# Kernel optimization log

Hardware: AMD Instinct MI355X
Metric: run time of the kernel (lower is better)

## Reference

```python
import jax, jax.numpy as jnp
import numpy as np

ORDER = 1024
U_SIZE = 128
Y_SIZE = 128
N_STEPS = 32768


def setup_inputs() -> dict:
    key = jax.random.key(0)
    k0, k1, k2, k3, k4 = jax.random.split(key, 5)
    inp = jax.random.normal(k0, (N_STEPS, U_SIZE), dtype=jnp.float32)
    # A scaled to spectral radius ~0.9 so the 32k-step recurrence is stable.
    A_w = jax.random.normal(k1, (ORDER, ORDER), dtype=jnp.float32) * (0.9 / np.sqrt(ORDER))
    B_w = jax.random.normal(k2, (ORDER, U_SIZE), dtype=jnp.float32) / np.sqrt(U_SIZE)
    C_w = jax.random.normal(k3, (Y_SIZE, ORDER), dtype=jnp.float32) / np.sqrt(ORDER)
    D_w = jax.random.normal(k4, (Y_SIZE, U_SIZE), dtype=jnp.float32) / np.sqrt(U_SIZE)
    return {"inp": inp, "A_w": A_w, "B_w": B_w, "C_w": C_w, "D_w": D_w}


def reference(inp, A_w, B_w, C_w, D_w):
    u_size = B_w.shape[1]
    order = A_w.shape[0]
    # Faithful to torch: input.reshape(u_size, -1), then column t is u at step t.
    us = inp.reshape(u_size, -1).T  # (N, u_size)
    x0 = jnp.zeros((order,), dtype=inp.dtype)

    def step(x, u):
        y = C_w @ x + D_w @ u          # (y_size,)
        x_next = A_w @ x + B_w @ u     # (order,)
        return x_next, y

    _, ys = jax.lax.scan(step, x0, us)
    return ys  # (N, y_size)
```

## Files before the change

kernel.cpp:

```cpp
#include <hip/hip_runtime.h>
#include <hip/hip_bf16.h>


#define NSTEPS 32768
#define LTRUNC 64
#define NDBLK  (LTRUNC + 1)
#define KTOT   (NDBLK * 128)
#define SPLITK 2

typedef __attribute__((ext_vector_type(8))) short short8;
typedef __attribute__((ext_vector_type(4))) float f32x4;
typedef __hip_bfloat16 bf16;

#define ME 1048576
#define O_AHR 0
#define O_ALR (1*ME)
#define O_AHC (2*ME)
#define O_ALC (3*ME)
#define O_XPH (4*ME)
#define O_XPL (5*ME)
#define O_XQH (6*ME)
#define O_XQL (7*ME)
#define O_YPH (8*ME)
#define O_YPL (9*ME)
#define O_YQH (10*ME)
#define O_YQL (11*ME)
#define O_GH  (12*ME)
#define O_GL  (14*ME)
#define O_RTH (16*ME)
#define O_RTL (O_RTH + 917504)
#define O_KBT (O_RTL + 917504)
#define O_UBF (O_KBT + 128*KTOT)

__device__ __forceinline__ void gload16(const void* g, void* l) {
  __builtin_amdgcn_global_load_lds(
      (const __attribute__((address_space(1))) void*)g,
      (__attribute__((address_space(3))) void*)l, 16, 0, 0);
}

__device__ __forceinline__ void split1(float x, bf16& h, bf16& l) {
  h = __float2bfloat16(x);
  l = __float2bfloat16(x - __bfloat162float(h));
}

__global__ __launch_bounds__(256) void prep(
    const float* __restrict__ inp, const float* __restrict__ Aw,
    const float* __restrict__ Bw, const float* __restrict__ Cw,
    const float* __restrict__ Dw, bf16* __restrict__ W, float* __restrict__ out)
{
  __shared__ float buf[128 * 65];
  const int tid = threadIdx.x;
  const int bid = blockIdx.x;

  if (bid < 512) {
    const int t0 = bid << 6;
#pragma unroll
    for (int i = 0; i < 32; ++i) {
      const int e = i * 256 + tid, sl = e >> 6, tl = e & 63;
      buf[sl * 65 + tl] = inp[(size_t)sl * NSTEPS + t0 + tl];
    }
    __syncthreads();
    bf16* Ubf = W + O_UBF;
#pragma unroll
    for (int i = 0; i < 32; ++i) {
      const int e = i * 256 + tid, tl = e >> 7, sl = e & 127;
      Ubf[(size_t)(LTRUNC + t0 + tl) * 128 + sl] = __float2bfloat16(buf[sl * 65 + tl]);
    }
  } else if (bid < 768) {
    const int base = (bid - 512) * 4096;
    bf16* hi = W + O_AHR; bf16* lo = W + O_ALR;
#pragma unroll
    for (int i = 0; i < 4; ++i) {
      const int e = base + i * 1024 + tid * 4;
      const float4 v = *reinterpret_cast<const float4*>(Aw + e);
      const float vv[4] = {v.x, v.y, v.z, v.w};
#pragma unroll
      for (int j = 0; j < 4; ++j) { bf16 h, l; split1(vv[j], h, l); hi[e+j] = h; lo[e+j] = l; }
    }
  } else if (bid < 1024) {
    const int idx = bid - 768;
    const int r0 = (idx >> 4) << 6, c0 = (idx & 15) << 6;
#pragma unroll
    for (int i = 0; i < 16; ++i) {
      const int e = i * 256 + tid, rl = e >> 6, cl = e & 63;
      buf[rl * 65 + cl] = Aw[(size_t)(r0 + rl) * 1024 + c0 + cl];
    }
    __syncthreads();
    bf16* hi = W + O_AHC; bf16* lo = W + O_ALC;
#pragma unroll
    for (int i = 0; i < 16; ++i) {
      const int e = i * 256 + tid, cl = e >> 6, rl = e & 63;
      bf16 h, l; split1(buf[rl * 65 + cl], h, l);
      hi[(size_t)(c0 + cl) * 1024 + r0 + rl] = h;
      lo[(size_t)(c0 + cl) * 1024 + r0 + rl] = l;
    }
  } else if (bid < 1056) {
    const int base = (bid - 1024) * 4096;
    bf16* hi = W + O_GH; bf16* lo = W + O_GL;
#pragma unroll
    for (int i = 0; i < 4; ++i) {
      const int e = base + i * 1024 + tid * 4;
      const float4 v = *reinterpret_cast<const float4*>(Cw + e);
      const float vv[4] = {v.x, v.y, v.z, v.w};
#pragma unroll
      for (int j = 0; j < 4; ++j) { bf16 h, l; split1(vv[j], h, l); hi[e+j] = h; lo[e+j] = l; }
    }
  } else if (bid < 1088) {
    const int idx = bid - 1056;
    const int r0 = (idx >> 1) << 6, c0 = (idx & 1) << 6;
#pragma unroll
    for (int i = 0; i < 16; ++i) {
      const int e = i * 256 + tid, rl = e >> 6, cl = e & 63;
      buf[rl * 65 + cl] = Bw[(size_t)(r0 + rl) * 128 + c0 + cl];
    }
    __syncthreads();
    bf16* hi = W + O_RTH; bf16* lo = W + O_RTL;
#pragma unroll
    for (int i = 0; i < 16; ++i) {
      const int e = i * 256 + tid, cl = e >> 6, rl = e & 63;
      bf16 h, l; split1(buf[rl * 65 + cl], h, l);
      hi[(size_t)(c0 + cl) * 1024 + r0 + rl] = h;
      lo[(size_t)(c0 + cl) * 1024 + r0 + rl] = l;
    }
  } else if (bid < 1092) {
    bf16* kb = W + O_KBT;
    const int e0 = (bid - 1088) * 4096 + tid * 16;
#pragma unroll
    for (int j = 0; j < 16; ++j) {
      const int e = e0 + j, r = e >> 7, s = e & 127;
      kb[(size_t)r * KTOT + s] = __float2bfloat16(Dw[e]);
    }
  } else if (bid < 1094) {
    bf16* Ubf = W + O_UBF;
    const int e = ((bid - 1092) * 256 + tid) * 16;
    short8 z = {0,0,0,0,0,0,0,0};
    *reinterpret_cast<short8*>(Ubf + e) = z;
    *reinterpret_cast<short8*>(Ubf + e + 8) = z;
  } else {
    float4* o4 = reinterpret_cast<float4*>(out);
    const int base = (bid - 1094) * 4096;
    const float4 z = {0.f, 0.f, 0.f, 0.f};
#pragma unroll
    for (int i = 0; i < 16; ++i) o4[base + i * 256 + tid] = z;
  }
}

struct Job { int ah, al, bh, bl, oh, ol, oth, otl, mt, nt, dbase; };
__device__ const Job JOBS[15] = {
  {O_AHR,O_ALR,O_AHC,O_ALC, O_XPH,O_XPL, O_YPH,O_YPL, 8,8,-1},
  {O_GH, O_GL, O_AHC,O_ALC, O_GH+131072,O_GL+131072, -1,-1, 1,8,-1},
  {O_XPH,O_XPL,O_YPH,O_YPL, O_XQH,O_XQL, O_YQH,O_YQL, 8,8,-1},
  {O_GH, O_GL, O_YPH,O_YPL, O_GH+262144,O_GL+262144, -1,-1, 2,8,-1},
  {O_XQH,O_XQL,O_YQH,O_YQL, O_XPH,O_XPL, O_YPH,O_YPL, 8,8,-1},
  {O_GH, O_GL, O_YQH,O_YQL, O_GH+524288,O_GL+524288, -1,-1, 4,8,-1},
  {O_XPH,O_XPL,O_YPH,O_YPL, O_XQH,O_XQL, O_YQH,O_YQL, 8,8,-1},
  {O_GH, O_GL, O_YPH,O_YPL, O_GH+1048576,O_GL+1048576, -1,-1, 8,8,-1},
  {O_XQH,O_XQL,O_YQH,O_YQL, O_XPH,O_XPL, -1,-1, 8,8,-1},
  {O_RTH,O_RTL,O_XQH,O_XQL, O_RTH+131072,O_RTL+131072, -1,-1, 1,8,-1},
  {O_GH,O_GL, O_RTH,        O_RTL,        O_KBT,0, -1,-1, 16,1, 1},
  {O_RTH,O_RTL,O_XPH,O_XPL, O_RTH+262144,O_RTL+262144, -1,-1, 2,8,-1},
  {O_GH,O_GL, O_RTH+131072, O_RTL+131072, O_KBT,0, -1,-1, 16,1, 17},
  {O_GH,O_GL, O_RTH+262144, O_RTL+262144, O_KBT,0, -1,-1, 16,1, 33},
  {O_GH,O_GL, O_RTH+393216, O_RTL+393216, O_KBT,0, -1,-1, 16,1, 49},
};
__device__ const int LVL[8] = {0,2,4,6,8,11,13,15};

__global__ __launch_bounds__(256) void chain_lvl(bf16* __restrict__ ws, int lvl)
{
  __shared__ __align__(16) char smem[131072];
  const int tid = threadIdx.x, lane = tid & 63, wave = tid >> 6;
  const int wm = wave & 1, wn = wave >> 1, l15 = lane & 15, lk = lane >> 4;
  const int srow = tid >> 3, sc8 = (tid & 7) << 3;
  const int g8 = (((tid & 7) ^ (srow & 7)) << 3);
  const int ca0 = ((lk ^ (l15 & 7)) << 3);
  const int ca1 = (((4 + lk) ^ (l15 & 7)) << 3);

  int idx = blockIdx.x;
  int j = LVL[lvl];
  const int je = LVL[lvl + 1];
  while (j < je && idx >= JOBS[j].mt * JOBS[j].nt) { idx -= JOBS[j].mt * JOBS[j].nt; ++j; }
  if (j >= je) return;
  const Job job = JOBS[j];
  const int my = idx / job.nt, nx = idx - my * job.nt;
  const int m0 = my << 7, n0 = nx << 7;
  const bf16* Ah = ws + job.ah; const bf16* Al = ws + job.al;
  const bf16* Bh = ws + job.bh; const bf16* Bl = ws + job.bl;
  f32x4 acc[4][4] = {};

  if (job.dbase >= 0) {
    auto stageK = [&](int ks, int buf) {
      char* base = smem + buf * 32768;
      const int k0 = ks << 6;
#pragma unroll
      for (int p = 0; p < 4; ++p) {
        const int row = (p << 5) + srow;
        const int loff = row * 128 + (sc8 << 1);
        gload16(Ah + (size_t)(m0 + row) * 1024 + k0 + g8, base + loff);
        gload16(Bh + (size_t)(n0 + row) * 1024 + k0 + g8, base + 16384 + loff);
      }
    };
    stageK(0, 0);
    for (int ks = 0; ks < 16; ++ks) {
      if (ks + 1 < 16) {
        stageK(ks + 1, (ks + 1) & 1);
        asm volatile("s_waitcnt vmcnt(8)" ::: "memory");
      } else {
        asm volatile("s_waitcnt vmcnt(0)" ::: "memory");
      }
      __builtin_amdgcn_s_barrier();
      __builtin_amdgcn_sched_barrier(0);
      {
        char* base = smem + (ks & 1) * 32768;
        const bf16* pAh = (const bf16*)(base);
        const bf16* pBh = (const bf16*)(base + 16384);
#pragma unroll
        for (int kh = 0; kh < 2; ++kh) {
          const int cb = kh ? ca1 : ca0;
          short8 ah[4], bh[4];
#pragma unroll
          for (int mi = 0; mi < 4; ++mi)
            ah[mi] = *reinterpret_cast<const short8*>(pAh + ((wm << 6) + (mi << 4) + l15) * 64 + cb);
#pragma unroll
          for (int ni = 0; ni < 4; ++ni)
            bh[ni] = *reinterpret_cast<const short8*>(pBh + ((wn << 6) + (ni << 4) + l15) * 64 + cb);
#pragma unroll
          for (int mi = 0; mi < 4; ++mi)
#pragma unroll
            for (int ni = 0; ni < 4; ++ni)
              acc[mi][ni] = __builtin_amdgcn_mfma_f32_16x16x32_bf16(ah[mi], bh[ni], acc[mi][ni], 0, 0, 0);
        }
      }
      __builtin_amdgcn_sched_barrier(0);
      __builtin_amdgcn_s_barrier();
    }
    bf16* kb = ws + job.oh;
    const int d = job.dbase + my;
#pragma unroll
    for (int mi = 0; mi < 4; ++mi)
#pragma unroll
      for (int ni = 0; ni < 4; ++ni) {
        const int cl = (wn << 6) + (ni << 4) + l15;
#pragma unroll
        for (int rg = 0; rg < 4; ++rg) {
          const int rl = (wm << 6) + (mi << 4) + (lk << 2) + rg;
          kb[(size_t)rl * KTOT + (size_t)d * 128 + cl] = __float2bfloat16(acc[mi][ni][rg]);
        }
      }
    return;
  }

  auto stage = [&](int ks, int buf) {
    char* base = smem + buf * 65536;
    const int k0 = ks << 6;
#pragma unroll
    for (int p = 0; p < 4; ++p) {
      const int row = (p << 5) + srow;
      const int loff = row * 128 + (sc8 << 1);
      const size_t aoff = (size_t)(m0 + row) * 1024 + k0 + g8;
      const size_t boff = (size_t)(n0 + row) * 1024 + k0 + g8;
      gload16(Ah + aoff, base + loff);
      gload16(Al + aoff, base + 16384 + loff);
      gload16(Bh + boff, base + 32768 + loff);
      gload16(Bl + boff, base + 49152 + loff);
    }
  };

  stage(0, 0);
  for (int ks = 0; ks < 16; ++ks) {
    if (ks + 1 < 16) {
      stage(ks + 1, (ks + 1) & 1);
      asm volatile("s_waitcnt vmcnt(16)" ::: "memory");
    } else {
      asm volatile("s_waitcnt vmcnt(0)" ::: "memory");
    }
    __builtin_amdgcn_s_barrier();
    __builtin_amdgcn_sched_barrier(0);
    {
      char* base = smem + (ks & 1) * 65536;
      const bf16* pAh = (const bf16*)(base);
      const bf16* pAl = (const bf16*)(base + 16384);
      const bf16* pBh = (const bf16*)(base + 32768);
      const bf16* pBl = (const bf16*)(base + 49152);
#pragma unroll
      for (int kh = 0; kh < 2; ++kh) {
        const int cb = kh ? ca1 : ca0;
        short8 ah[4], al[4], bh[4], bl[4];
#pragma unroll
        for (int mi = 0; mi < 4; ++mi) {
          const int r = ((wm << 6) + (mi << 4) + l15) * 64 + cb;
          ah[mi] = *reinterpret_cast<const short8*>(pAh + r);
          al[mi] = *reinterpret_cast<const short8*>(pAl + r);
        }
#pragma unroll
        for (int ni = 0; ni < 4; ++ni) {
          const int r = ((wn << 6) + (ni << 4) + l15) * 64 + cb;
          bh[ni] = *reinterpret_cast<const short8*>(pBh + r);
          bl[ni] = *reinterpret_cast<const short8*>(pBl + r);
        }
#pragma unroll
        for (int mi = 0; mi < 4; ++mi)
#pragma unroll
          for (int ni = 0; ni < 4; ++ni) {
            acc[mi][ni] = __builtin_amdgcn_mfma_f32_16x16x32_bf16(ah[mi], bh[ni], acc[mi][ni], 0, 0, 0);
            acc[mi][ni] = __builtin_amdgcn_mfma_f32_16x16x32_bf16(ah[mi], bl[ni], acc[mi][ni], 0, 0, 0);
            acc[mi][ni] = __builtin_amdgcn_mfma_f32_16x16x32_bf16(al[mi], bh[ni], acc[mi][ni], 0, 0, 0);
          }
      }
    }
    __builtin_amdgcn_sched_barrier(0);
    __builtin_amdgcn_s_barrier();
  }

  {
    bf16* oh = ws + job.oh; bf16* ol = ws + job.ol;
#pragma unroll
    for (int mi = 0; mi < 4; ++mi)
#pragma unroll
      for (int ni = 0; ni < 4; ++ni) {
        const int cl = (wn << 6) + (ni << 4) + l15;
#pragma unroll
        for (int rg = 0; rg < 4; ++rg) {
          const int rl = (wm << 6) + (mi << 4) + (lk << 2) + rg;
          bf16 h, l; split1(acc[mi][ni][rg], h, l);
          oh[(size_t)(m0 + rl) * 1024 + n0 + cl] = h;
          ol[(size_t)(m0 + rl) * 1024 + n0 + cl] = l;
        }
      }
    if (job.oth >= 0) {
      float* tT = (float*)smem;
      __syncthreads();
#pragma unroll
      for (int mi = 0; mi < 4; ++mi)
#pragma unroll
        for (int ni = 0; ni < 4; ++ni) {
          const int cl = (wn << 6) + (ni << 4) + l15;
#pragma unroll
          for (int rg = 0; rg < 4; ++rg) {
            const int rl = (wm << 6) + (mi << 4) + (lk << 2) + rg;
            tT[rl * 129 + cl] = acc[mi][ni][rg];
          }
        }
      __syncthreads();
      bf16* yh = ws + job.oth; bf16* yl = ws + job.otl;
#pragma unroll
      for (int i = 0; i < 64; ++i) {
        const int e = i * 256 + tid, yr = e >> 7, yc = e & 127;
        bf16 h, l; split1(tT[yc * 129 + yr], h, l);
        yh[(size_t)(n0 + yr) * 1024 + m0 + yc] = h;
        yl[(size_t)(n0 + yr) * 1024 + m0 + yc] = l;
      }
    }
  }
}

__global__ __launch_bounds__(256) void conv_mfma(
    const bf16* __restrict__ Ubf, const bf16* __restrict__ Kbt, float* __restrict__ out)
{
  __shared__ __align__(16) char smem[73728];
  const int tid = threadIdx.x;
  const int t0 = blockIdx.x << 7;
  const int y = blockIdx.y;
  const int lane = tid & 63, wave = tid >> 6;
  const int wm = wave & 1, wn = wave >> 1;
  const int l15 = lane & 15, lk = lane >> 4;
  const int srow = tid >> 3, sc8 = (tid & 7) << 3;
  const int g8 = (((tid & 7) ^ (srow & 7)) << 3);
  const int ca0 = ((lk ^ (l15 & 7)) << 3);
  const int ca1 = (((4 + lk) ^ (l15 & 7)) << 3);
  const int d_hi = y ? LTRUNC : 32;
  const int sb = y ? 66 : 0, se = y ? 130 : 66;
  bf16* U = (bf16*)smem;
  bf16* Bs0 = (bf16*)(smem + 40960);
  bf16* Bs1 = (bf16*)(smem + 57344);
  f32x4 acc[4][4] = {};

  const long u0 = (long)LTRUNC + t0 - d_hi;
#pragma unroll
  for (int i = 0; i < 10; ++i) {
    const int idx = i * 256 + tid;
    const int r = idx >> 4, c = idx & 15;
    gload16(Ubf + (size_t)(u0 + r) * 128 + ((c ^ (r & 15)) << 3), smem + idx * 16);
  }

  auto stageB = [&](int it, bf16* Bbuf) {
    const int kk0 = it << 6;
#pragma unroll
    for (int p = 0; p < 4; ++p) {
      const int row = (p << 5) + srow;
      gload16(Kbt + (size_t)row * KTOT + kk0 + g8, Bbuf + row * 64 + sc8);
    }
  };

  stageB(sb, Bs0);
  int cur = 0;
  for (int it = sb; it < se; ++it) {
    if (it + 1 < se) {
      stageB(it + 1, cur ? Bs0 : Bs1);
      asm volatile("s_waitcnt vmcnt(4)" ::: "memory");
    } else {
      asm volatile("s_waitcnt vmcnt(0)" ::: "memory");
    }
    __builtin_amdgcn_s_barrier();
    __builtin_amdgcn_sched_barrier(0);
    {
      const bf16* Bcur = cur ? Bs1 : Bs0;
      const int d = it >> 1;
      const int dhd = d_hi - d;
      const int cbase = (it & 1) << 3;
#pragma unroll
      for (int kh = 0; kh < 2; ++kh) {
        short8 a[4], b[4];
#pragma unroll
        for (int mi = 0; mi < 4; ++mi) {
          const int row = dhd + (wm << 6) + (mi << 4) + l15;
          const int ch = (cbase + (kh << 2) + lk) ^ (row & 15);
          a[mi] = *reinterpret_cast<const short8*>(U + row * 128 + (ch << 3));
        }
        const int cb = kh ? ca1 : ca0;
#pragma unroll
        for (int ni = 0; ni < 4; ++ni)
          b[ni] = *reinterpret_cast<const short8*>(Bcur + ((wn << 6) + (ni << 4) + l15) * 64 + cb);
#pragma unroll
        for (int mi = 0; mi < 4; ++mi)
#pragma unroll
          for (int ni = 0; ni < 4; ++ni)
            acc[mi][ni] = __builtin_amdgcn_mfma_f32_16x16x32_bf16(a[mi], b[ni], acc[mi][ni], 0, 0, 0);
      }
    }
    __builtin_amdgcn_sched_barrier(0);
    __builtin_amdgcn_s_barrier();
    cur ^= 1;
  }
#pragma unroll
  for (int mi = 0; mi < 4; ++mi)
#pragma unroll
    for (int ni = 0; ni < 4; ++ni) {
      const int rcol = (wn << 6) + (ni << 4) + l15;
#pragma unroll
      for (int rg = 0; rg < 4; ++rg) {
        const int t = t0 + (wm << 6) + (mi << 4) + (lk << 2) + rg;
        atomicAdd(out + (size_t)t * 128 + rcol, acc[mi][ni][rg]);
      }
    }
}

extern "C" void kernel_launch(void* const* d_in, const int* in_sizes, int n_in,
                              void* d_out, int out_size, void* d_ws, size_t ws_size,
                              hipStream_t stream)
{
  const float* inp = (const float*)d_in[0];
  const float* Aw  = (const float*)d_in[1];
  const float* Bw  = (const float*)d_in[2];
  const float* Cw  = (const float*)d_in[3];
  const float* Dw  = (const float*)d_in[4];
  float* out = (float*)d_out;
  (void)in_sizes; (void)n_in; (void)out_size; (void)ws_size;

  bf16* W = (bf16*)d_ws;

  prep<<<1350, 256, 0, stream>>>(inp, Aw, Bw, Cw, Dw, W, out);

  const int lvl_wgs[7] = {72, 80, 96, 128, 88, 32, 32};
  for (int lvl = 0; lvl < 7; ++lvl)
    chain_lvl<<<lvl_wgs[lvl], 256, 0, stream>>>(W, lvl);

  conv_mfma<<<dim3(NSTEPS / 128, SPLITK), 256, 0, stream>>>(W + O_UBF, W + O_KBT, out);
}
```

Measured before the change: 294.8 us.

## Switch GEMM and conv kernels to 4-stage K=32 pipeline with single barrier

In all three MFMA loops (chain_lvl K-only path, chain_lvl split-precision path, conv_mfma), the double-buffered K=64 tiles become a four-buffer ring of K=32 tiles with three stages prefetched ahead. Each iteration now uses a single barrier placed before the next prefetch instead of two, and a new XOR swizzle matches the 32-wide rows. The aim is deeper latency hiding and fewer barriers per MFMA. The cost is twice as many iterations with less MFMA work each, plus more complex waitcnt bookkeeping in the tail.

```diff
diff --git a/kernel.cpp b/kernel.cpp
--- a/kernel.cpp
+++ b/kernel.cpp
@@ -170,10 +170,7 @@
   __shared__ __align__(16) char smem[131072];
   const int tid = threadIdx.x, lane = tid & 63, wave = tid >> 6;
   const int wm = wave & 1, wn = wave >> 1, l15 = lane & 15, lk = lane >> 4;
-  const int srow = tid >> 3, sc8 = (tid & 7) << 3;
-  const int g8 = (((tid & 7) ^ (srow & 7)) << 3);
-  const int ca0 = ((lk ^ (l15 & 7)) << 3);
-  const int ca1 = (((4 + lk) ^ (l15 & 7)) << 3);
+  const int cswz = lk ^ ((l15 >> 1) & 3);
 
   int idx = blockIdx.x;
   int j = LVL[lvl];
@@ -188,50 +185,52 @@
   f32x4 acc[4][4] = {};
 
   if (job.dbase >= 0) {
-    auto stageK = [&](int ks, int buf) {
-      char* base = smem + buf * 32768;
-      const int k0 = ks << 6;
-#pragma unroll
-      for (int p = 0; p < 4; ++p) {
-        const int row = (p << 5) + srow;
-        const int loff = row * 128 + (sc8 << 1);
-        gload16(Ah + (size_t)(m0 + row) * 1024 + k0 + g8, base + loff);
-        gload16(Bh + (size_t)(n0 + row) * 1024 + k0 + g8, base + 16384 + loff);
+    auto stageK = [&](int s) {
+      char* base = smem + (s & 3) * 32768;
+      const int k0 = s << 5;
+#pragma unroll
+      for (int q8 = 0; q8 < 2; ++q8) {
+        const int q = q8 * 256 + tid;
+        const int row = q >> 2, c = q & 3;
+        const int src = k0 + ((c ^ ((row >> 1) & 3)) << 3);
+        gload16(Ah + (size_t)(m0 + row) * 1024 + src, base + q * 16);
+        gload16(Bh + (size_t)(n0 + row) * 1024 + src, base + 8192 + q * 16);
       }
     };
-    stageK(0, 0);
-    for (int ks = 0; ks < 16; ++ks) {
-      if (ks + 1 < 16) {
-        stageK(ks + 1, (ks + 1) & 1);
+    stageK(0); stageK(1); stageK(2);
+    for (int ks = 0; ks < 32; ++ks) {
+      if (ks + 3 < 32) {
         asm volatile("s_waitcnt vmcnt(8)" ::: "memory");
+        __builtin_amdgcn_s_barrier();
+        stageK(ks + 3);
+      } else if (ks + 2 < 32) {
+        asm volatile("s_waitcnt vmcnt(8)" ::: "memory");
+        __builtin_amdgcn_s_barrier();
+      } else if (ks + 1 < 32) {
+        asm volatile("s_waitcnt vmcnt(4)" ::: "memory");
+        __builtin_amdgcn_s_barrier();
       } else {
         asm volatile("s_waitcnt vmcnt(0)" ::: "memory");
-      }
-      __builtin_amdgcn_s_barrier();
+        __builtin_amdgcn_s_barrier();
+      }
       __builtin_amdgcn_sched_barrier(0);
       {
-        char* base = smem + (ks & 1) * 32768;
+        char* base = smem + (ks & 3) * 32768;
         const bf16* pAh = (const bf16*)(base);
-        const bf16* pBh = (const bf16*)(base + 16384);
-#pragma unroll
-        for (int kh = 0; kh < 2; ++kh) {
-          const int cb = kh ? ca1 : ca0;
-          short8 ah[4], bh[4];
-#pragma unroll
-          for (int mi = 0; mi < 4; ++mi)
-            ah[mi] = *reinterpret_cast<const short8*>(pAh + ((wm << 6) + (mi << 4) + l15) * 64 + cb);
+        const bf16* pBh = (const bf16*)(base + 8192);
+        short8 ah[4], bh[4];
+#pragma unroll
+        for (int mi = 0; mi < 4; ++mi)
+          ah[mi] = *reinterpret_cast<const short8*>(pAh + ((wm << 6) + (mi << 4) + l15) * 32 + (cswz << 3));
+#pragma unroll
+        for (int ni = 0; ni < 4; ++ni)
+          bh[ni] = *reinterpret_cast<const short8*>(pBh + ((wn << 6) + (ni << 4) + l15) * 32 + (cswz << 3));
+#pragma unroll
+        for (int mi = 0; mi < 4; ++mi)
 #pragma unroll
           for (int ni = 0; ni < 4; ++ni)
-            bh[ni] = *reinterpret_cast<const short8*>(pBh + ((wn << 6) + (ni << 4) + l15) * 64 + cb);
-#pragma unroll
-          for (int mi = 0; mi < 4; ++mi)
-#pragma unroll
-            for (int ni = 0; ni < 4; ++ni)
-              acc[mi][ni] = __builtin_amdgcn_mfma_f32_16x16x32_bf16(ah[mi], bh[ni], acc[mi][ni], 0, 0, 0);
-        }
-      }
-      __builtin_amdgcn_sched_barrier(0);
-      __builtin_amdgcn_s_barrier();
+            acc[mi][ni] = __builtin_amdgcn_mfma_f32_16x16x32_bf16(ah[mi], bh[ni], acc[mi][ni], 0, 0, 0);
+      }
     }
     bf16* kb = ws + job.oh;
     const int d = job.dbase + my;
@@ -249,66 +248,68 @@
     return;
   }
 
-  auto stage = [&](int ks, int buf) {
-    char* base = smem + buf * 65536;
-    const int k0 = ks << 6;
-#pragma unroll
-    for (int p = 0; p < 4; ++p) {
-      const int row = (p << 5) + srow;
-      const int loff = row * 128 + (sc8 << 1);
-      const size_t aoff = (size_t)(m0 + row) * 1024 + k0 + g8;
-      const size_t boff = (size_t)(n0 + row) * 1024 + k0 + g8;
-      gload16(Ah + aoff, base + loff);
-      gload16(Al + aoff, base + 16384 + loff);
-      gload16(Bh + boff, base + 32768 + loff);
-      gload16(Bl + boff, base + 49152 + loff);
+  auto stage = [&](int s) {
+    char* base = smem + (s & 3) * 32768;
+    const int k0 = s << 5;
+#pragma unroll
+    for (int q8 = 0; q8 < 2; ++q8) {
+      const int q = q8 * 256 + tid;
+      const int row = q >> 2, c = q & 3;
+      const int src = k0 + ((c ^ ((row >> 1) & 3)) << 3);
+      const size_t aoff = (size_t)(m0 + row) * 1024 + src;
+      const size_t boff = (size_t)(n0 + row) * 1024 + src;
+      gload16(Ah + aoff, base + q * 16);
+      gload16(Al + aoff, base + 8192 + q * 16);
+      gload16(Bh + boff, base + 16384 + q * 16);
+      gload16(Bl + boff, base + 24576 + q * 16);
     }
   };
 
-  stage(0, 0);
-  for (int ks = 0; ks < 16; ++ks) {
-    if (ks + 1 < 16) {
-      stage(ks + 1, (ks + 1) & 1);
+  stage(0); stage(1); stage(2);
+  for (int ks = 0; ks < 32; ++ks) {
+    if (ks + 3 < 32) {
       asm volatile("s_waitcnt vmcnt(16)" ::: "memory");
+      __builtin_amdgcn_s_barrier();
+      stage(ks + 3);
+    } else if (ks + 2 < 32) {
+      asm volatile("s_waitcnt vmcnt(16)" ::: "memory");
+      __builtin_amdgcn_s_barrier();
+    } else if (ks + 1 < 32) {
+      asm volatile("s_waitcnt vmcnt(8)" ::: "memory");
+      __builtin_amdgcn_s_barrier();
     } else {
       asm volatile("s_waitcnt vmcnt(0)" ::: "memory");
-    }
-    __builtin_amdgcn_s_barrier();
+      __builtin_amdgcn_s_barrier();
+    }
     __builtin_amdgcn_sched_barrier(0);
     {
-      char* base = smem + (ks & 1) * 65536;
+      char* base = smem + (ks & 3) * 32768;
       const bf16* pAh = (const bf16*)(base);
-      const bf16* pAl = (const bf16*)(base + 16384);
-      const bf16* pBh = (const bf16*)(base + 32768);
-      const bf16* pBl = (const bf16*)(base + 49152);
-#pragma unroll
-      for (int kh = 0; kh < 2; ++kh) {
-        const int cb = kh ? ca1 : ca0;
-        short8 ah[4], al[4], bh[4], bl[4];
-#pragma unroll
-        for (int mi = 0; mi < 4; ++mi) {
-          const int r = ((wm << 6) + (mi << 4) + l15) * 64 + cb;
-          ah[mi] = *reinterpret_cast<const short8*>(pAh + r);
-          al[mi] = *reinterpret_cast<const short8*>(pAl + r);
+      const bf16* pAl = (const bf16*)(base + 8192);
+      const bf16* pBh = (const bf16*)(base + 16384);
+      const bf16* pBl = (const bf16*)(base + 24576);
+      short8 ah[4], al[4], bh[4], bl[4];
+#pragma unroll
+      for (int mi = 0; mi < 4; ++mi) {
+        const int r = ((wm << 6) + (mi << 4) + l15) * 32 + (cswz << 3);
+        ah[mi] = *reinterpret_cast<const short8*>(pAh + r);
+        al[mi] = *reinterpret_cast<const short8*>(pAl + r);
+      }
+#pragma unroll
+      for (int ni = 0; ni < 4; ++ni) {
+        const int r = ((wn << 6) + (ni << 4) + l15) * 32 + (cswz << 3);
+        bh[ni] = *reinterpret_cast<const short8*>(pBh + r);
+        bl[ni] = *reinterpret_cast<const short8*>(pBl + r);
+      }
+#pragma unroll
+      for (int mi = 0; mi < 4; ++mi)
+#pragma unroll
+        for (int ni = 0; ni < 4; ++ni) {
+          acc[mi][ni] = __builtin_amdgcn_mfma_f32_16x16x32_bf16(ah[mi], bh[ni], acc[mi][ni], 0, 0, 0);
+          acc[mi][ni] = __builtin_amdgcn_mfma_f32_16x16x32_bf16(ah[mi], bl[ni], acc[mi][ni], 0, 0, 0);
+          acc[mi][ni] = __builtin_amdgcn_mfma_f32_16x16x32_bf16(al[mi], bh[ni], acc[mi][ni], 0, 0, 0);
         }
-#pragma unroll
-        for (int ni = 0; ni < 4; ++ni) {
-          const int r = ((wn << 6) + (ni << 4) + l15) * 64 + cb;
-          bh[ni] = *reinterpret_cast<const short8*>(pBh + r);
-          bl[ni] = *reinterpret_cast<const short8*>(pBl + r);
-        }
-#pragma unroll
-        for (int mi = 0; mi < 4; ++mi)
-#pragma unroll
-          for (int ni = 0; ni < 4; ++ni) {
-            acc[mi][ni] = __builtin_amdgcn_mfma_f32_16x16x32_bf16(ah[mi], bh[ni], acc[mi][ni], 0, 0, 0);
-            acc[mi][ni] = __builtin_amdgcn_mfma_f32_16x16x32_bf16(ah[mi], bl[ni], acc[mi][ni], 0, 0, 0);
-            acc[mi][ni] = __builtin_amdgcn_mfma_f32_16x16x32_bf16(al[mi], bh[ni], acc[mi][ni], 0, 0, 0);
-          }
-      }
-    }
-    __builtin_amdgcn_sched_barrier(0);
-    __builtin_amdgcn_s_barrier();
+    }
   }
 
   {
@@ -363,15 +364,10 @@
   const int lane = tid & 63, wave = tid >> 6;
   const int wm = wave & 1, wn = wave >> 1;
   const int l15 = lane & 15, lk = lane >> 4;
-  const int srow = tid >> 3, sc8 = (tid & 7) << 3;
-  const int g8 = (((tid & 7) ^ (srow & 7)) << 3);
-  const int ca0 = ((lk ^ (l15 & 7)) << 3);
-  const int ca1 = (((4 + lk) ^ (l15 & 7)) << 3);
+  const int cswz = lk ^ ((l15 >> 1) & 3);
   const int d_hi = y ? LTRUNC : 32;
-  const int sb = y ? 66 : 0, se = y ? 130 : 66;
+  const int sb = y ? 132 : 0, se = y ? 260 : 132;
   bf16* U = (bf16*)smem;
-  bf16* Bs0 = (bf16*)(smem + 40960);
-  bf16* Bs1 = (bf16*)(smem + 57344);
   f32x4 acc[4][4] = {};
 
   const long u0 = (long)LTRUNC + t0 - d_hi;
@@ -382,54 +378,55 @@
     gload16(Ubf + (size_t)(u0 + r) * 128 + ((c ^ (r & 15)) << 3), smem + idx * 16);
   }
 
-  auto stageB = [&](int it, bf16* Bbuf) {
-    const int kk0 = it << 6;
-#pragma unroll
-    for (int p = 0; p < 4; ++p) {
-      const int row = (p << 5) + srow;
-      gload16(Kbt + (size_t)row * KTOT + kk0 + g8, Bbuf + row * 64 + sc8);
+  auto stageB = [&](int it2) {
+    bf16* Bbuf = (bf16*)(smem + 40960 + (it2 & 3) * 8192);
+    const size_t kbase = (size_t)(it2 >> 2) * 128 + ((it2 & 3) << 5);
+#pragma unroll
+    for (int q8 = 0; q8 < 2; ++q8) {
+      const int q = q8 * 256 + tid;
+      const int row = q >> 2, c = q & 3;
+      gload16(Kbt + (size_t)row * KTOT + kbase + ((c ^ ((row >> 1) & 3)) << 3),
+              (char*)Bbuf + q * 16);
     }
   };
 
-  stageB(sb, Bs0);
-  int cur = 0;
+  stageB(sb); stageB(sb + 1); stageB(sb + 2);
   for (int it = sb; it < se; ++it) {
-    if (it + 1 < se) {
-      stageB(it + 1, cur ? Bs0 : Bs1);
+    if (it + 3 < se) {
       asm volatile("s_waitcnt vmcnt(4)" ::: "memory");
+      __builtin_amdgcn_s_barrier();
+      stageB(it + 3);
+    } else if (it + 2 < se) {
+      asm volatile("s_waitcnt vmcnt(4)" ::: "memory");
+      __builtin_amdgcn_s_barrier();
+    } else if (it + 1 < se) {
+      asm volatile("s_waitcnt vmcnt(2)" ::: "memory");
+      __builtin_amdgcn_s_barrier();
     } else {
       asm volatile("s_waitcnt vmcnt(0)" ::: "memory");
-    }
-    __builtin_amdgcn_s_barrier();
+      __builtin_amdgcn_s_barrier();
+    }
     __builtin_amdgcn_sched_barrier(0);
     {
-      const bf16* Bcur = cur ? Bs1 : Bs0;
-      const int d = it >> 1;
+      const bf16* Bcur = (const bf16*)(smem + 40960 + (it & 3) * 8192);
+      const int d = it >> 2;
       const int dhd = d_hi - d;
-      const int cbase = (it & 1) << 3;
-#pragma unroll
-      for (int kh = 0; kh < 2; ++kh) {
-        short8 a[4], b[4];
-#pragma unroll
-        for (int mi = 0; mi < 4; ++mi) {
-          const int row = dhd + (wm << 6) + (mi << 4) + l15;
-          const int ch = (cbase + (kh << 2) + lk) ^ (row & 15);
-          a[mi] = *reinterpret_cast<const short8*>(U + row * 128 + (ch << 3));
-        }
-        const int cb = kh ? ca1 : ca0;
+      const int chu = (((it & 3) << 2) | lk) ^ ((dhd + l15) & 15);
+      short8 a[4], b[4];
+#pragma unroll
+      for (int mi = 0; mi < 4; ++mi) {
+        const int row = dhd + (wm << 6) + (mi << 4) + l15;
+        a[mi] = *reinterpret_cast<const short8*>(U + row * 128 + (chu << 3));
+      }
+#pragma unroll
+      for (int ni = 0; ni < 4; ++ni)
+        b[ni] = *reinterpret_cast<const short8*>(Bcur + ((wn << 6) + (ni << 4) + l15) * 32 + (cswz << 3));
+#pragma unroll
+      for (int mi = 0; mi < 4; ++mi)
 #pragma unroll
         for (int ni = 0; ni < 4; ++ni)
-          b[ni] = *reinterpret_cast<const short8*>(Bcur + ((wn << 6) + (ni << 4) + l15) * 64 + cb);
-#pragma unroll
-        for (int mi = 0; mi < 4; ++mi)
-#pragma unroll
-          for (int ni = 0; ni < 4; ++ni)
-            acc[mi][ni] = __builtin_amdgcn_mfma_f32_16x16x32_bf16(a[mi], b[ni], acc[mi][ni], 0, 0, 0);
-      }
-    }
-    __builtin_amdgcn_sched_barrier(0);
-    __builtin_amdgcn_s_barrier();
-    cur ^= 1;
+          acc[mi][ni] = __builtin_amdgcn_mfma_f32_16x16x32_bf16(a[mi], b[ni], acc[mi][ni], 0, 0, 0);
+    }
   }
 #pragma unroll
   for (int mi = 0; mi < 4; ++mi)
```

Result: faster. 273.7 us (-7.2%).
